# Kernel tuning notes

Measured on AMD Instinct MI355X. Metric: run time of the kernel, lower is better.

## Reference

```python
import jax, jax.numpy as jnp
import numpy as np

B = 2048
C = 32            # num_categories
STATE_DIM = 64    # state_input_dim
EMB = 256         # emb_dim
OUT = 256         # output_dim
OBS_DIM = 512


def _cat_linear(x, W_all, b_all, cat_ids):
    # x: [B,S,din]; W_all: [C,din,dout]; b_all: [C,dout]; cat_ids: [B]
    W = W_all[cat_ids]            # [B,din,dout]  (per-sample weight gather)
    b = b_all[cat_ids]            # [B,dout]
    return jnp.einsum('bsd,bdh->bsh', x, W) + b[:, None, :]


def setup_inputs() -> dict:
    key = jax.random.key(0)
    ks = jax.random.split(key, 8)
    state = jax.random.normal(ks[0], (B, STATE_DIM), dtype=jnp.float32)
    obs = jax.random.uniform(ks[1], (B, 1, OBS_DIM), dtype=jnp.float32)
    cat_ids = jax.random.randint(ks[2], (B,), 0, C)
    obs_W = 0.01 * jax.random.normal(ks[3], (OBS_DIM, EMB), dtype=jnp.float32)
    obs_b = jnp.zeros((EMB,), dtype=jnp.float32)
    state_W = 0.02 * jax.random.normal(ks[4], (C, STATE_DIM, EMB), dtype=jnp.float32)
    state_b = jnp.zeros((C, EMB), dtype=jnp.float32)
    l2_W = 0.02 * jax.random.normal(ks[5], (C, 2 * EMB, OUT), dtype=jnp.float32)
    l2_b = jnp.zeros((C, OUT), dtype=jnp.float32)
    return {"state": state, "obs": obs, "cat_ids": cat_ids,
            "obs_W": obs_W, "obs_b": obs_b,
            "state_W": state_W, "state_b": state_b,
            "l2_W": l2_W, "l2_b": l2_b}


def reference(state, obs, cat_ids, obs_W, obs_b, state_W, state_b, l2_W, l2_b):
    # ObsEncoder (modeled as a linear projection): [B,1,OBS_DIM] -> [B,1,EMB]
    obs_emb = jnp.einsum('bsd,dh->bsh', obs, obs_W) + obs_b
    # state: [B,STATE_DIM] -> [B,1,STATE_DIM]
    state3 = state[:, None, :]
    state_emb = jax.nn.relu(_cat_linear(state3, state_W, state_b, cat_ids))  # [B,1,EMB]
    x = jnp.concatenate((state_emb, obs_emb), axis=2)                        # [B,1,2*EMB]
    return _cat_linear(x, l2_W, l2_b, cat_ids)                               # [B,1,OUT]
```

## Files before the change

kernel.cpp:

```cpp
#include <hip/hip_runtime.h>

constexpr int B_N   = 2048;
constexpr int C_N   = 32;
constexpr int SD    = 64;
constexpr int EMB   = 256;
constexpr int OUTD  = 256;
constexpr int OBSD  = 512;
constexpr int XDIM  = 512;
constexpr int CAP   = 256;

typedef __attribute__((ext_vector_type(8))) short bf16x8;
typedef __attribute__((ext_vector_type(4))) short bf16x4;
typedef __attribute__((ext_vector_type(4))) float f32x4;

constexpr size_t OFF_ROWS  = 4096;
constexpr size_t OFF_POBS  = 65536;
constexpr size_t OFF_PSTAT = 327680;
constexpr size_t OFF_PL2   = 1376256;
constexpr size_t NEED_L2   = OFF_PL2 + (size_t)C_N * XDIM * OUTD * 2;

__device__ __forceinline__ unsigned short bf_cvt(float f) {
    union { float f; unsigned u; } x; x.f = f;
    unsigned r = x.u + 0x7FFF + ((x.u >> 16) & 1);
    return (unsigned short)(r >> 16);
}

__global__ __launch_bounds__(256) void prep_kernel(
    const int* __restrict__ cat_ids,
    const float* __restrict__ obs_W, const float* __restrict__ state_W,
    const float* __restrict__ l2_W,
    int* __restrict__ counts, int* __restrict__ rows,
    unsigned short* __restrict__ p_obs, unsigned short* __restrict__ p_state,
    unsigned short* __restrict__ p_l2, int do_l2) {
    const int bid = blockIdx.x;
    const int t = threadIdx.x;

    if (bid < C_N) {
        __shared__ int cnt;
        __shared__ int list[CAP];
        if (t == 0) cnt = 0;
        __syncthreads();
        const int c = bid;
        for (int r = t; r < B_N; r += 256) {
            if (cat_ids[r] == c) {
                int s = atomicAdd(&cnt, 1);
                if (s < CAP) list[s] = r;
            }
        }
        __syncthreads();
        int n = min(cnt, CAP);
        for (int s = t; s < n; s += 256) rows[c * CAP + s] = list[s];
        if (t == 0) counts[c] = n;
        return;
    }

    const float* src;
    unsigned short* dst;
    {
        int pb = bid - C_N;
        if (pb < 16) {
            src = obs_W + (size_t)pb * 32 * 256;
            dst = p_obs + (size_t)pb * 8192;
        } else if (pb < 80) {
            int i = pb - 16;
            int mat = i >> 1, ch = i & 1;
            src = state_W + ((size_t)mat * SD + ch * 32) * 256;
            dst = p_state + (size_t)i * 8192;
        } else {
            if (!do_l2) return;
            int i = pb - 80;
            int mat = i >> 4, ch = i & 15;
            src = l2_W + ((size_t)mat * XDIM + ch * 32) * 256;
            dst = p_l2 + (size_t)i * 8192;
        }
    }

    __shared__ __align__(16) unsigned short sW[32 * 264];
    #pragma unroll
    for (int i2 = 0; i2 < 8; ++i2) {
        int f = t + 256 * i2;
        int row = f >> 6, c4 = f & 63;
        float4 v = ((const float4*)src)[f];
        unsigned short* d = &sW[row * 264 + c4 * 4];
        d[0] = bf_cvt(v.x); d[1] = bf_cvt(v.y); d[2] = bf_cvt(v.z); d[3] = bf_cvt(v.w);
    }
    __syncthreads();
    #pragma unroll
    for (int s4 = 0; s4 < 4; ++s4) {
        int slot = s4 * 256 + t;
        int strip = slot >> 6, lane = slot & 63;
        int r0 = (lane >> 4) * 8, col = strip * 16 + (lane & 15);
        unsigned short v[8];
        #pragma unroll
        for (int j = 0; j < 8; ++j) v[j] = sW[(r0 + j) * 264 + col];
        *(bf16x8*)(dst + (size_t)slot * 8) = *(bf16x8*)v;
    }
}

__global__ __launch_bounds__(512) void fused_kernel(
    const float* __restrict__ state, const float* __restrict__ obs,
    const float* __restrict__ obs_b, const float* __restrict__ state_b,
    const float* __restrict__ l2_W, const float* __restrict__ l2_b,
    const int* __restrict__ counts, const int* __restrict__ rows,
    const unsigned short* __restrict__ p_obs,
    const unsigned short* __restrict__ p_state,
    const unsigned short* __restrict__ p_l2, int has_pl2,
    float* __restrict__ out) {
    const int c = blockIdx.x;
    const int tile = blockIdx.y;
    const int n = counts[c];
    const int rbase = tile * 16;
    if (rbase >= n) return;
    const int nr = min(16, n - rbase);

    __shared__ __align__(16) unsigned short sAs[16 * 72];
    __shared__ __align__(16) unsigned short sAo[16 * 520];
    __shared__ __align__(16) unsigned short sX[16 * 520];
    __shared__ int sRows[16];

    const int t = threadIdx.x;
    const int w = t >> 6, l = t & 63;
    const int ml = l & 15, quad = l >> 4;

    if (t < 16) sRows[t] = (t < nr) ? rows[c * CAP + rbase + t] : 0;

    const bf16x8* pb1 = (const bf16x8*)(p_state + (size_t)c * SD * 256);
    const bf16x8* pb2 = (const bf16x8*)p_obs;
    bf16x8 pf1[4], pf2[12];
    #pragma unroll
    for (int kk = 0; kk < 2; ++kk)
        #pragma unroll
        for (int si = 0; si < 2; ++si)
            pf1[kk * 2 + si] = pb1[(kk * 16 + w * 2 + si) * 64 + l];
    #pragma unroll
    for (int kk = 0; kk < 6; ++kk)
        #pragma unroll
        for (int si = 0; si < 2; ++si)
            pf2[kk * 2 + si] = pb2[(kk * 16 + w * 2 + si) * 64 + l];

    __syncthreads();

    if (t < 256) {
        int i = t >> 4, c4 = t & 15;
        unsigned short vv[4] = {0, 0, 0, 0};
        if (i < nr) {
            float4 v = ((const float4*)(state + (size_t)sRows[i] * SD))[c4];
            vv[0] = bf_cvt(v.x); vv[1] = bf_cvt(v.y); vv[2] = bf_cvt(v.z); vv[3] = bf_cvt(v.w);
        }
        *(bf16x4*)&sAs[i * 72 + c4 * 4] = *(bf16x4*)vv;
    }
    #pragma unroll
    for (int i2 = 0; i2 < 4; ++i2) {
        int f = t + 512 * i2;
        int i = f >> 7, c4 = f & 127;
        unsigned short vv[4] = {0, 0, 0, 0};
        if (i < nr) {
            float4 v = ((const float4*)(obs + (size_t)sRows[i] * OBSD))[c4];
            vv[0] = bf_cvt(v.x); vv[1] = bf_cvt(v.y); vv[2] = bf_cvt(v.z); vv[3] = bf_cvt(v.w);
        }
        *(bf16x4*)&sAo[i * 520 + c4 * 4] = *(bf16x4*)vv;
    }
    __syncthreads();

    {
        f32x4 acc[2];
        #pragma unroll
        for (int si = 0; si < 2; ++si) acc[si] = (f32x4){0.f, 0.f, 0.f, 0.f};
        #pragma unroll
        for (int kk = 0; kk < 2; ++kk) {
            bf16x8 a = *(const bf16x8*)&sAs[ml * 72 + kk * 32 + quad * 8];
            #pragma unroll
            for (int si = 0; si < 2; ++si)
                acc[si] = __builtin_amdgcn_mfma_f32_16x16x32_bf16(a, pf1[kk * 2 + si], acc[si], 0, 0, 0);
        }
        #pragma unroll
        for (int si = 0; si < 2; ++si) {
            int colb = (w * 2 + si) * 16 + ml;
            float bias = state_b[c * 256 + colb];
            #pragma unroll
            for (int r = 0; r < 4; ++r)
                sX[(quad * 4 + r) * 520 + colb] = bf_cvt(fmaxf(acc[si][r] + bias, 0.f));
        }
    }

    {
        f32x4 acc[2];
        #pragma unroll
        for (int si = 0; si < 2; ++si) acc[si] = (f32x4){0.f, 0.f, 0.f, 0.f};
        #pragma unroll
        for (int kk = 0; kk < 16; ++kk) {
            bf16x8 a = *(const bf16x8*)&sAo[ml * 520 + kk * 32 + quad * 8];
            #pragma unroll
            for (int si = 0; si < 2; ++si) {
                int slot = (kk % 6) * 2 + si;
                bf16x8 b = pf2[slot];
                if (kk < 10)
                    pf2[slot] = pb2[((kk + 6) * 16 + w * 2 + si) * 64 + l];
                acc[si] = __builtin_amdgcn_mfma_f32_16x16x32_bf16(a, b, acc[si], 0, 0, 0);
            }
        }
        #pragma unroll
        for (int si = 0; si < 2; ++si) {
            int colb = (w * 2 + si) * 16 + ml;
            float bias = obs_b[colb];
            #pragma unroll
            for (int r = 0; r < 4; ++r)
                sX[(quad * 4 + r) * 520 + 256 + colb] = bf_cvt(acc[si][r] + bias);
        }
    }

    const bf16x8* pb3 = (const bf16x8*)p_l2 + (size_t)c * 16384;
    bf16x8 pf3[12];
    if (has_pl2) {
        #pragma unroll
        for (int kk = 0; kk < 6; ++kk)
            #pragma unroll
            for (int si = 0; si < 2; ++si)
                pf3[kk * 2 + si] = pb3[(kk * 16 + w * 2 + si) * 64 + l];
    }
    __syncthreads();

    {
        f32x4 acc[2];
        #pragma unroll
        for (int si = 0; si < 2; ++si) acc[si] = (f32x4){0.f, 0.f, 0.f, 0.f};
        if (has_pl2) {
            #pragma unroll
            for (int kk = 0; kk < 16; ++kk) {
                bf16x8 a = *(const bf16x8*)&sX[ml * 520 + kk * 32 + quad * 8];
                #pragma unroll
                for (int si = 0; si < 2; ++si) {
                    int slot = (kk % 6) * 2 + si;
                    bf16x8 b = pf3[slot];
                    if (kk < 10)
                        pf3[slot] = pb3[((kk + 6) * 16 + w * 2 + si) * 64 + l];
                    acc[si] = __builtin_amdgcn_mfma_f32_16x16x32_bf16(a, b, acc[si], 0, 0, 0);
                }
            }
        } else {
            for (int kk = 0; kk < 16; ++kk) {
                bf16x8 a = *(const bf16x8*)&sX[ml * 520 + kk * 32 + quad * 8];
                #pragma unroll
                for (int si = 0; si < 2; ++si) {
                    const float* wsrc = l2_W + ((size_t)c * XDIM + kk * 32 + quad * 8) * 256
                                        + (w * 2 + si) * 16 + ml;
                    bf16x8 b;
                    #pragma unroll
                    for (int j = 0; j < 8; ++j) b[j] = (short)bf_cvt(wsrc[j * 256]);
                    acc[si] = __builtin_amdgcn_mfma_f32_16x16x32_bf16(a, b, acc[si], 0, 0, 0);
                }
            }
        }
        #pragma unroll
        for (int si = 0; si < 2; ++si) {
            int colb = (w * 2 + si) * 16 + ml;
            float bias = l2_b[c * 256 + colb];
            #pragma unroll
            for (int r = 0; r < 4; ++r) {
                int row = quad * 4 + r;
                if (row < nr)
                    out[(size_t)sRows[row] * 256 + colb] = acc[si][r] + bias;
            }
        }
    }
}

extern "C" void kernel_launch(void* const* d_in, const int* in_sizes, int n_in,
                              void* d_out, int out_size, void* d_ws, size_t ws_size,
                              hipStream_t stream) {
    const float* state   = (const float*)d_in[0];
    const float* obs     = (const float*)d_in[1];
    const int*   cat_ids = (const int*)d_in[2];
    const float* obs_W   = (const float*)d_in[3];
    const float* obs_b   = (const float*)d_in[4];
    const float* state_W = (const float*)d_in[5];
    const float* state_b = (const float*)d_in[6];
    const float* l2_W    = (const float*)d_in[7];
    const float* l2_b    = (const float*)d_in[8];
    float* out = (float*)d_out;

    char* ws = (char*)d_ws;
    int* counts  = (int*)ws;
    int* rowsbuf = (int*)(ws + OFF_ROWS);
    unsigned short* p_obs  = (unsigned short*)(ws + OFF_POBS);
    unsigned short* p_stat = (unsigned short*)(ws + OFF_PSTAT);
    unsigned short* p_l2   = (unsigned short*)(ws + OFF_PL2);
    const int do_l2 = (ws_size >= NEED_L2) ? 1 : 0;

    int prep_blocks = C_N + 16 + 64 + (do_l2 ? 512 : 0);
    prep_kernel<<<dim3(prep_blocks), dim3(256), 0, stream>>>(
        cat_ids, obs_W, state_W, l2_W, counts, rowsbuf, p_obs, p_stat, p_l2, do_l2);

    fused_kernel<<<dim3(C_N, CAP / 16), dim3(512), 0, stream>>>(
        state, obs, obs_b, state_b, l2_W, l2_b, counts, rowsbuf,
        p_obs, p_stat, p_l2, do_l2, out);
}
```

Before: 98.22 us.

## Fuse bucketing and weight conversion into single kernel, drop prep pass

Removes the separate prep kernel that bucketed rows by category and pre-packed all weights into bf16 MFMA fragments. Each block now computes its own row list with wave ballots and prefix sums over cat_ids, and loads fp32 weights directly from global memory, converting them to bf16 in registers with a three-stage rolling prefetch. This drops one kernel launch and the write and re-read of packed weights. In exchange, every tile block redoes the cat_ids scan and the per-element fp32 weight conversion, and the weight loads are strided and uncoalesced. Tiles are capped at 16 per category, which silently drops rows if a category holds more than 256.

```diff
diff --git a/kernel.cpp b/kernel.cpp
--- a/kernel.cpp
+++ b/kernel.cpp
@@ -1,266 +1,196 @@
 #include <hip/hip_runtime.h>
 
-constexpr int B_N   = 2048;
 constexpr int C_N   = 32;
 constexpr int SD    = 64;
-constexpr int EMB   = 256;
-constexpr int OUTD  = 256;
 constexpr int OBSD  = 512;
-constexpr int XDIM  = 512;
-constexpr int CAP   = 256;
+constexpr int TILES = 16;
 
 typedef __attribute__((ext_vector_type(8))) short bf16x8;
-typedef __attribute__((ext_vector_type(4))) short bf16x4;
 typedef __attribute__((ext_vector_type(4))) float f32x4;
 
-constexpr size_t OFF_ROWS  = 4096;
-constexpr size_t OFF_POBS  = 65536;
-constexpr size_t OFF_PSTAT = 327680;
-constexpr size_t OFF_PL2   = 1376256;
-constexpr size_t NEED_L2   = OFF_PL2 + (size_t)C_N * XDIM * OUTD * 2;
+union Frag { unsigned u[4]; bf16x8 h; };
 
 __device__ __forceinline__ unsigned short bf_cvt(float f) {
     union { float f; unsigned u; } x; x.f = f;
-    unsigned r = x.u + 0x7FFF + ((x.u >> 16) & 1);
+    unsigned r = x.u + 0x7FFFu + ((x.u >> 16) & 1u);
     return (unsigned short)(r >> 16);
 }
-
-__global__ __launch_bounds__(256) void prep_kernel(
+__device__ __forceinline__ unsigned bf_pack2(float a, float b) {
+    union { float f; unsigned u; } x, y; x.f = a; y.f = b;
+    unsigned ra = x.u + 0x7FFFu + ((x.u >> 16) & 1u);
+    unsigned rb = y.u + 0x7FFFu + ((y.u >> 16) & 1u);
+    return (ra >> 16) | (rb & 0xFFFF0000u);
+}
+
+#define LOADB(DST, WP, K0) { const float* _p = (WP) + (size_t)((K0) + quad * 8) * 256 + wcol; \
+    _Pragma("unroll") for (int _j = 0; _j < 8; ++_j) { (DST)[_j] = _p[_j * 256]; (DST)[8 + _j] = _p[_j * 256 + 16]; } }
+
+#define PACKLO(F, S) { (F).u[0] = bf_pack2((S)[0], (S)[1]);  (F).u[1] = bf_pack2((S)[2], (S)[3]); \
+                       (F).u[2] = bf_pack2((S)[4], (S)[5]);  (F).u[3] = bf_pack2((S)[6], (S)[7]); }
+#define PACKHI(F, S) { (F).u[0] = bf_pack2((S)[8], (S)[9]);  (F).u[1] = bf_pack2((S)[10], (S)[11]); \
+                       (F).u[2] = bf_pack2((S)[12], (S)[13]); (F).u[3] = bf_pack2((S)[14], (S)[15]); }
+
+__global__ __launch_bounds__(512, 2) void fused_kernel(
+    const float* __restrict__ state, const float* __restrict__ obs,
     const int* __restrict__ cat_ids,
-    const float* __restrict__ obs_W, const float* __restrict__ state_W,
-    const float* __restrict__ l2_W,
-    int* __restrict__ counts, int* __restrict__ rows,
-    unsigned short* __restrict__ p_obs, unsigned short* __restrict__ p_state,
-    unsigned short* __restrict__ p_l2, int do_l2) {
-    const int bid = blockIdx.x;
-    const int t = threadIdx.x;
-
-    if (bid < C_N) {
-        __shared__ int cnt;
-        __shared__ int list[CAP];
-        if (t == 0) cnt = 0;
-        __syncthreads();
-        const int c = bid;
-        for (int r = t; r < B_N; r += 256) {
-            if (cat_ids[r] == c) {
-                int s = atomicAdd(&cnt, 1);
-                if (s < CAP) list[s] = r;
-            }
-        }
-        __syncthreads();
-        int n = min(cnt, CAP);
-        for (int s = t; s < n; s += 256) rows[c * CAP + s] = list[s];
-        if (t == 0) counts[c] = n;
-        return;
-    }
-
-    const float* src;
-    unsigned short* dst;
-    {
-        int pb = bid - C_N;
-        if (pb < 16) {
-            src = obs_W + (size_t)pb * 32 * 256;
-            dst = p_obs + (size_t)pb * 8192;
-        } else if (pb < 80) {
-            int i = pb - 16;
-            int mat = i >> 1, ch = i & 1;
-            src = state_W + ((size_t)mat * SD + ch * 32) * 256;
-            dst = p_state + (size_t)i * 8192;
-        } else {
-            if (!do_l2) return;
-            int i = pb - 80;
-            int mat = i >> 4, ch = i & 15;
-            src = l2_W + ((size_t)mat * XDIM + ch * 32) * 256;
-            dst = p_l2 + (size_t)i * 8192;
-        }
-    }
-
-    __shared__ __align__(16) unsigned short sW[32 * 264];
-    #pragma unroll
-    for (int i2 = 0; i2 < 8; ++i2) {
-        int f = t + 256 * i2;
-        int row = f >> 6, c4 = f & 63;
-        float4 v = ((const float4*)src)[f];
-        unsigned short* d = &sW[row * 264 + c4 * 4];
-        d[0] = bf_cvt(v.x); d[1] = bf_cvt(v.y); d[2] = bf_cvt(v.z); d[3] = bf_cvt(v.w);
-    }
-    __syncthreads();
-    #pragma unroll
-    for (int s4 = 0; s4 < 4; ++s4) {
-        int slot = s4 * 256 + t;
-        int strip = slot >> 6, lane = slot & 63;
-        int r0 = (lane >> 4) * 8, col = strip * 16 + (lane & 15);
-        unsigned short v[8];
-        #pragma unroll
-        for (int j = 0; j < 8; ++j) v[j] = sW[(r0 + j) * 264 + col];
-        *(bf16x8*)(dst + (size_t)slot * 8) = *(bf16x8*)v;
-    }
-}
-
-__global__ __launch_bounds__(512) void fused_kernel(
-    const float* __restrict__ state, const float* __restrict__ obs,
-    const float* __restrict__ obs_b, const float* __restrict__ state_b,
+    const float* __restrict__ obs_W, const float* __restrict__ obs_b,
+    const float* __restrict__ state_W, const float* __restrict__ state_b,
     const float* __restrict__ l2_W, const float* __restrict__ l2_b,
-    const int* __restrict__ counts, const int* __restrict__ rows,
-    const unsigned short* __restrict__ p_obs,
-    const unsigned short* __restrict__ p_state,
-    const unsigned short* __restrict__ p_l2, int has_pl2,
     float* __restrict__ out) {
+
     const int c = blockIdx.x;
     const int tile = blockIdx.y;
-    const int n = counts[c];
+    const int t = threadIdx.x;
+    const int w = t >> 6, l = t & 63;
+    const int ml = l & 15, quad = l >> 4;
+    const int wcol = w * 32 + ml;
+
+    __shared__ int scnt[32];
+    __shared__ int sbase[33];
+    __shared__ int sRows[16];
+    __shared__ __align__(16) unsigned short sAs[16 * 72];
+    __shared__ __align__(16) unsigned short sAo[16 * 520];
+    __shared__ __align__(16) unsigned short sX[16 * 520];
+
+    unsigned long long mym[4];
+    #pragma unroll
+    for (int i = 0; i < 4; ++i) {
+        int r = t + 512 * i;
+        unsigned long long bal = __ballot(cat_ids[r] == c);
+        mym[i] = bal;
+        if (l == 0) scnt[w + 8 * i] = __popcll(bal);
+    }
+    __syncthreads();
+    if (t == 0) {
+        int run = 0;
+        for (int j = 0; j < 32; ++j) { sbase[j] = run; run += scnt[j]; }
+        sbase[32] = run;
+    }
+    __syncthreads();
+    const int n = sbase[32];
     const int rbase = tile * 16;
     if (rbase >= n) return;
     const int nr = min(16, n - rbase);
 
-    __shared__ __align__(16) unsigned short sAs[16 * 72];
-    __shared__ __align__(16) unsigned short sAo[16 * 520];
-    __shared__ __align__(16) unsigned short sX[16 * 520];
-    __shared__ int sRows[16];
-
-    const int t = threadIdx.x;
-    const int w = t >> 6, l = t & 63;
-    const int ml = l & 15, quad = l >> 4;
-
-    if (t < 16) sRows[t] = (t < nr) ? rows[c * CAP + rbase + t] : 0;
-
-    const bf16x8* pb1 = (const bf16x8*)(p_state + (size_t)c * SD * 256);
-    const bf16x8* pb2 = (const bf16x8*)p_obs;
-    bf16x8 pf1[4], pf2[12];
-    #pragma unroll
-    for (int kk = 0; kk < 2; ++kk)
-        #pragma unroll
-        for (int si = 0; si < 2; ++si)
-            pf1[kk * 2 + si] = pb1[(kk * 16 + w * 2 + si) * 64 + l];
-    #pragma unroll
-    for (int kk = 0; kk < 6; ++kk)
-        #pragma unroll
-        for (int si = 0; si < 2; ++si)
-            pf2[kk * 2 + si] = pb2[(kk * 16 + w * 2 + si) * 64 + l];
-
+    const float* pbs = state_W + (size_t)c * SD * 256;
+    float r10[16], r11[16], rb0[16], rb1[16], rb2[16];
+    LOADB(r10, pbs, 0)
+    LOADB(r11, pbs, 32)
+    LOADB(rb0, obs_W, 0)
+    LOADB(rb1, obs_W, 32)
+    LOADB(rb2, obs_W, 64)
+
+    const int colb0 = wcol, colb1 = wcol + 16;
+    const float bs0 = state_b[c * 256 + colb0], bs1 = state_b[c * 256 + colb1];
+    const float bo0 = obs_b[colb0],             bo1 = obs_b[colb1];
+    const float bl0 = l2_b[c * 256 + colb0],    bl1 = l2_b[c * 256 + colb1];
+
+    const unsigned long long ltm = (l == 0) ? 0ull : (~0ull >> (64 - l));
+    #pragma unroll
+    for (int i = 0; i < 4; ++i) {
+        if ((mym[i] >> l) & 1ull) {
+            int s = sbase[w + 8 * i] + __popcll(mym[i] & ltm) - rbase;
+            if (s >= 0 && s < 16) sRows[s] = t + 512 * i;
+        }
+    }
     __syncthreads();
 
     if (t < 256) {
         int i = t >> 4, c4 = t & 15;
-        unsigned short vv[4] = {0, 0, 0, 0};
+        uint2 vv = make_uint2(0u, 0u);
         if (i < nr) {
             float4 v = ((const float4*)(state + (size_t)sRows[i] * SD))[c4];
-            vv[0] = bf_cvt(v.x); vv[1] = bf_cvt(v.y); vv[2] = bf_cvt(v.z); vv[3] = bf_cvt(v.w);
-        }
-        *(bf16x4*)&sAs[i * 72 + c4 * 4] = *(bf16x4*)vv;
+            vv.x = bf_pack2(v.x, v.y); vv.y = bf_pack2(v.z, v.w);
+        }
+        *(uint2*)&sAs[i * 72 + c4 * 4] = vv;
     }
     #pragma unroll
     for (int i2 = 0; i2 < 4; ++i2) {
         int f = t + 512 * i2;
         int i = f >> 7, c4 = f & 127;
-        unsigned short vv[4] = {0, 0, 0, 0};
+        uint2 vv = make_uint2(0u, 0u);
         if (i < nr) {
             float4 v = ((const float4*)(obs + (size_t)sRows[i] * OBSD))[c4];
-            vv[0] = bf_cvt(v.x); vv[1] = bf_cvt(v.y); vv[2] = bf_cvt(v.z); vv[3] = bf_cvt(v.w);
-        }
-        *(bf16x4*)&sAo[i * 520 + c4 * 4] = *(bf16x4*)vv;
+            vv.x = bf_pack2(v.x, v.y); vv.y = bf_pack2(v.z, v.w);
+        }
+        *(uint2*)&sAo[i * 520 + c4 * 4] = vv;
     }
     __syncthreads();
 
     {
-        f32x4 acc[2];
+        f32x4 acc0 = {0.f, 0.f, 0.f, 0.f}, acc1 = {0.f, 0.f, 0.f, 0.f};
+        bf16x8 a0 = *(const bf16x8*)&sAs[ml * 72 + quad * 8];
+        bf16x8 a1 = *(const bf16x8*)&sAs[ml * 72 + 32 + quad * 8];
+        Frag f0, f1;
+        PACKLO(f0, r10) PACKHI(f1, r10)
+        acc0 = __builtin_amdgcn_mfma_f32_16x16x32_bf16(a0, f0.h, acc0, 0, 0, 0);
+        acc1 = __builtin_amdgcn_mfma_f32_16x16x32_bf16(a0, f1.h, acc1, 0, 0, 0);
+        PACKLO(f0, r11) PACKHI(f1, r11)
+        acc0 = __builtin_amdgcn_mfma_f32_16x16x32_bf16(a1, f0.h, acc0, 0, 0, 0);
+        acc1 = __builtin_amdgcn_mfma_f32_16x16x32_bf16(a1, f1.h, acc1, 0, 0, 0);
         #pragma unroll
-        for (int si = 0; si < 2; ++si) acc[si] = (f32x4){0.f, 0.f, 0.f, 0.f};
-        #pragma unroll
-        for (int kk = 0; kk < 2; ++kk) {
-            bf16x8 a = *(const bf16x8*)&sAs[ml * 72 + kk * 32 + quad * 8];
-            #pragma unroll
-            for (int si = 0; si < 2; ++si)
-                acc[si] = __builtin_amdgcn_mfma_f32_16x16x32_bf16(a, pf1[kk * 2 + si], acc[si], 0, 0, 0);
-        }
-        #pragma unroll
-        for (int si = 0; si < 2; ++si) {
-            int colb = (w * 2 + si) * 16 + ml;
-            float bias = state_b[c * 256 + colb];
-            #pragma unroll
-            for (int r = 0; r < 4; ++r)
-                sX[(quad * 4 + r) * 520 + colb] = bf_cvt(fmaxf(acc[si][r] + bias, 0.f));
-        }
-    }
-
+        for (int r = 0; r < 4; ++r) {
+            sX[(quad * 4 + r) * 520 + colb0] = bf_cvt(fmaxf(acc0[r] + bs0, 0.f));
+            sX[(quad * 4 + r) * 520 + colb1] = bf_cvt(fmaxf(acc1[r] + bs1, 0.f));
+        }
+    }
+
+    f32x4 acc[2];
+    acc[0] = (f32x4){0.f, 0.f, 0.f, 0.f};
+    acc[1] = (f32x4){0.f, 0.f, 0.f, 0.f};
     {
-        f32x4 acc[2];
-        #pragma unroll
-        for (int si = 0; si < 2; ++si) acc[si] = (f32x4){0.f, 0.f, 0.f, 0.f};
-        #pragma unroll
-        for (int kk = 0; kk < 16; ++kk) {
-            bf16x8 a = *(const bf16x8*)&sAo[ml * 520 + kk * 32 + quad * 8];
-            #pragma unroll
-            for (int si = 0; si < 2; ++si) {
-                int slot = (kk % 6) * 2 + si;
-                bf16x8 b = pf2[slot];
-                if (kk < 10)
-                    pf2[slot] = pb2[((kk + 6) * 16 + w * 2 + si) * 64 + l];
-                acc[si] = __builtin_amdgcn_mfma_f32_16x16x32_bf16(a, b, acc[si], 0, 0, 0);
-            }
-        }
-        #pragma unroll
-        for (int si = 0; si < 2; ++si) {
-            int colb = (w * 2 + si) * 16 + ml;
-            float bias = obs_b[colb];
-            #pragma unroll
-            for (int r = 0; r < 4; ++r)
-                sX[(quad * 4 + r) * 520 + 256 + colb] = bf_cvt(acc[si][r] + bias);
-        }
-    }
-
-    const bf16x8* pb3 = (const bf16x8*)p_l2 + (size_t)c * 16384;
-    bf16x8 pf3[12];
-    if (has_pl2) {
-        #pragma unroll
-        for (int kk = 0; kk < 6; ++kk)
-            #pragma unroll
-            for (int si = 0; si < 2; ++si)
-                pf3[kk * 2 + si] = pb3[(kk * 16 + w * 2 + si) * 64 + l];
-    }
-    __syncthreads();
-
+        Frag f0, f1;
+        #define P2STEP(KK, RB) { \
+            bf16x8 a = *(const bf16x8*)&sAo[ml * 520 + (KK) * 32 + quad * 8]; \
+            PACKLO(f0, RB) PACKHI(f1, RB) \
+            if ((KK) + 3 < 16) LOADB(RB, obs_W, ((KK) + 3) * 32) \
+            acc[0] = __builtin_amdgcn_mfma_f32_16x16x32_bf16(a, f0.h, acc[0], 0, 0, 0); \
+            acc[1] = __builtin_amdgcn_mfma_f32_16x16x32_bf16(a, f1.h, acc[1], 0, 0, 0); }
+        P2STEP(0,  rb0) P2STEP(1,  rb1) P2STEP(2,  rb2)
+        P2STEP(3,  rb0) P2STEP(4,  rb1) P2STEP(5,  rb2)
+        P2STEP(6,  rb0) P2STEP(7,  rb1) P2STEP(8,  rb2)
+        P2STEP(9,  rb0) P2STEP(10, rb1) P2STEP(11, rb2)
+        P2STEP(12, rb0) P2STEP(13, rb1) P2STEP(14, rb2)
+        P2STEP(15, rb0)
+        #undef P2STEP
+    }
+
+    const float* pb3 = l2_W + (size_t)c * 512 * 256;
+    LOADB(rb0, pb3, 0)
+    LOADB(rb1, pb3, 32)
+    LOADB(rb2, pb3, 64)
+    #pragma unroll
+    for (int r = 0; r < 4; ++r) {
+        sX[(quad * 4 + r) * 520 + 256 + colb0] = bf_cvt(acc[0][r] + bo0);
+        sX[(quad * 4 + r) * 520 + 256 + colb1] = bf_cvt(acc[1][r] + bo1);
+    }
+    __syncthreads();
+
+    acc[0] = (f32x4){0.f, 0.f, 0.f, 0.f};
+    acc[1] = (f32x4){0.f, 0.f, 0.f, 0.f};
     {
-        f32x4 acc[2];
-        #pragma unroll
-        for (int si = 0; si < 2; ++si) acc[si] = (f32x4){0.f, 0.f, 0.f, 0.f};
-        if (has_pl2) {
-            #pragma unroll
-            for (int kk = 0; kk < 16; ++kk) {
-                bf16x8 a = *(const bf16x8*)&sX[ml * 520 + kk * 32 + quad * 8];
-                #pragma unroll
-                for (int si = 0; si < 2; ++si) {
-                    int slot = (kk % 6) * 2 + si;
-                    bf16x8 b = pf3[slot];
-                    if (kk < 10)
-                        pf3[slot] = pb3[((kk + 6) * 16 + w * 2 + si) * 64 + l];
-                    acc[si] = __builtin_amdgcn_mfma_f32_16x16x32_bf16(a, b, acc[si], 0, 0, 0);
-                }
-            }
-        } else {
-            for (int kk = 0; kk < 16; ++kk) {
-                bf16x8 a = *(const bf16x8*)&sX[ml * 520 + kk * 32 + quad * 8];
-                #pragma unroll
-                for (int si = 0; si < 2; ++si) {
-                    const float* wsrc = l2_W + ((size_t)c * XDIM + kk * 32 + quad * 8) * 256
-                                        + (w * 2 + si) * 16 + ml;
-                    bf16x8 b;
-                    #pragma unroll
-                    for (int j = 0; j < 8; ++j) b[j] = (short)bf_cvt(wsrc[j * 256]);
-                    acc[si] = __builtin_amdgcn_mfma_f32_16x16x32_bf16(a, b, acc[si], 0, 0, 0);
-                }
-            }
-        }
-        #pragma unroll
-        for (int si = 0; si < 2; ++si) {
-            int colb = (w * 2 + si) * 16 + ml;
-            float bias = l2_b[c * 256 + colb];
-            #pragma unroll
-            for (int r = 0; r < 4; ++r) {
-                int row = quad * 4 + r;
-                if (row < nr)
-                    out[(size_t)sRows[row] * 256 + colb] = acc[si][r] + bias;
-            }
+        Frag f0, f1;
+        #define P3STEP(KK, RB) { \
+            bf16x8 a = *(const bf16x8*)&sX[ml * 520 + (KK) * 32 + quad * 8]; \
+            PACKLO(f0, RB) PACKHI(f1, RB) \
+            if ((KK) + 3 < 16) LOADB(RB, pb3, ((KK) + 3) * 32) \
+            acc[0] = __builtin_amdgcn_mfma_f32_16x16x32_bf16(a, f0.h, acc[0], 0, 0, 0); \
+            acc[1] = __builtin_amdgcn_mfma_f32_16x16x32_bf16(a, f1.h, acc[1], 0, 0, 0); }
+        P3STEP(0,  rb0) P3STEP(1,  rb1) P3STEP(2,  rb2)
+        P3STEP(3,  rb0) P3STEP(4,  rb1) P3STEP(5,  rb2)
+        P3STEP(6,  rb0) P3STEP(7,  rb1) P3STEP(8,  rb2)
+        P3STEP(9,  rb0) P3STEP(10, rb1) P3STEP(11, rb2)
+        P3STEP(12, rb0) P3STEP(13, rb1) P3STEP(14, rb2)
+        P3STEP(15, rb0)
+        #undef P3STEP
+    }
+    #pragma unroll
+    for (int r = 0; r < 4; ++r) {
+        int row = quad * 4 + r;
+        if (row < nr) {
+            float* orow = out + (size_t)sRows[row] * 256;
+            orow[colb0] = acc[0][r] + bl0;
+            orow[colb1] = acc[1][r] + bl1;
         }
     }
 }
@@ -268,30 +198,16 @@
 extern "C" void kernel_launch(void* const* d_in, const int* in_sizes, int n_in,
                               void* d_out, int out_size, void* d_ws, size_t ws_size,
                               hipStream_t stream) {
-    const float* state   = (const float*)d_in[0];
-    const float* obs     = (const float*)d_in[1];
-    const int*   cat_ids = (const int*)d_in[2];
-    const float* obs_W   = (const float*)d_in[3];
-    const float* obs_b   = (const float*)d_in[4];
-    const float* state_W = (const float*)d_in[5];
-    const float* state_b = (const float*)d_in[6];
-    const float* l2_W    = (const float*)d_in[7];
-    const float* l2_b    = (const float*)d_in[8];
-    float* out = (float*)d_out;
-
-    char* ws = (char*)d_ws;
-    int* counts  = (int*)ws;
-    int* rowsbuf = (int*)(ws + OFF_ROWS);
-    unsigned short* p_obs  = (unsigned short*)(ws + OFF_POBS);
-    unsigned short* p_stat = (unsigned short*)(ws + OFF_PSTAT);
-    unsigned short* p_l2   = (unsigned short*)(ws + OFF_PL2);
-    const int do_l2 = (ws_size >= NEED_L2) ? 1 : 0;
-
-    int prep_blocks = C_N + 16 + 64 + (do_l2 ? 512 : 0);
-    prep_kernel<<<dim3(prep_blocks), dim3(256), 0, stream>>>(
-        cat_ids, obs_W, state_W, l2_W, counts, rowsbuf, p_obs, p_stat, p_l2, do_l2);
-
-    fused_kernel<<<dim3(C_N, CAP / 16), dim3(512), 0, stream>>>(
-        state, obs, obs_b, state_b, l2_W, l2_b, counts, rowsbuf,
-        p_obs, p_stat, p_l2, do_l2, out);
-}
+    (void)in_sizes; (void)n_in; (void)out_size; (void)d_ws; (void)ws_size;
+    fused_kernel<<<dim3(C_N, TILES), dim3(512), 0, stream>>>(
+        (const float*)d_in[0],
+        (const float*)d_in[1],
+        (const int*)d_in[2],
+        (const float*)d_in[3],
+        (const float*)d_in[4],
+        (const float*)d_in[5],
+        (const float*)d_in[6],
+        (const float*)d_in[7],
+        (const float*)d_in[8],
+        (float*)d_out);
+}
```

New measurement: 98.80 us. No clear change (+0.6%).
